# Performance work log

Measured on AMD Instinct MI355X. Metric: run time of the kernel, lower is better.

## Reference

```python
import jax, jax.numpy as jnp
import numpy as np

HIDDEN = 5120
HEAD_DIM = 128
HQ = 40
HKV = 8
NUM_MOD = 3
Q_SIZE = HQ * HEAD_DIM          # 5120
KV_SIZE = HKV * HEAD_DIM        # 1024
GATE = HQ                       # attn gating enabled
QKV_OUT = Q_SIZE + 2 * KV_SIZE + GATE  # 7208
EPS = 1e-6
N_TOK = 2048


def setup_inputs() -> dict:
    key = jax.random.key(0)
    ks = jax.random.split(key, 8)
    s = 0.02
    return {
        "hidden_states": jax.random.normal(ks[0], (N_TOK, HIDDEN), jnp.float32),
        "rope": jax.random.normal(ks[1], (N_TOK, HEAD_DIM), jnp.float32),
        "pre_norm_w": jax.random.normal(ks[2], (NUM_MOD * HIDDEN,), jnp.float32) * s,
        "qkv_w": jax.random.normal(ks[3], (NUM_MOD * QKV_OUT, HIDDEN), jnp.float32) * s,
        "q_norm_w": jax.random.normal(ks[4], (NUM_MOD * HEAD_DIM,), jnp.float32) * s,
        "k_norm_w": jax.random.normal(ks[5], (NUM_MOD * HEAD_DIM,), jnp.float32) * s,
        "proj_w": jax.random.normal(ks[6], (NUM_MOD * HIDDEN, Q_SIZE), jnp.float32) * s,
        "modality_ids": jax.random.randint(ks[7], (N_TOK,), 0, NUM_MOD, jnp.int64),
    }


def _mm_rmsnorm(x, w_flat, mids, dim):
    # per-token modality weight slice; residual parameterization (w + 1)
    w = w_flat.reshape(NUM_MOD, dim)[mids]  # [N, dim]
    if x.ndim == 3:
        w = w[:, None, :]  # broadcast over heads
    rms = jax.lax.rsqrt(jnp.mean(x * x, axis=-1, keepdims=True) + EPS)
    return x * rms * (w + 1.0)


def _moe_linear(x, w_flat, mids, out_f):
    # 3 GEMMs (one per expert), then per-token select -- same math as masked dispatch
    wm = w_flat.reshape(NUM_MOD, out_f, x.shape[-1])
    outs = jnp.einsum('nd,mod->nmo', x, wm)  # [N, 3, out_f]
    return jnp.take_along_axis(outs, mids[:, None, None], axis=1)[:, 0, :]


def _rotary(x, cos, sin):
    # x: [N, H, D]; cos/sin: [N, D/2]
    x1, x2 = jnp.split(x, 2, axis=-1)
    c = cos[:, None, :]
    s = sin[:, None, :]
    return jnp.concatenate([x1 * c - x2 * s, x1 * s + x2 * c], axis=-1)


def reference(hidden_states, rope, pre_norm_w, qkv_w, q_norm_w, k_norm_w, proj_w, modality_ids):
    N = hidden_states.shape[0]
    mids = modality_ids

    h = _mm_rmsnorm(hidden_states, pre_norm_w, mids, HIDDEN)
    qkv = _moe_linear(h, qkv_w, mids, QKV_OUT)  # [N, 7208]
    q, k, v, g = jnp.split(qkv, [Q_SIZE, Q_SIZE + KV_SIZE, Q_SIZE + 2 * KV_SIZE], axis=-1)
    q = q.reshape(N, HQ, HEAD_DIM)
    k = k.reshape(N, HKV, HEAD_DIM)
    v = v.reshape(N, HKV, HEAD_DIM)

    q = _mm_rmsnorm(q, q_norm_w, mids, HEAD_DIM)
    k = _mm_rmsnorm(k, k_norm_w, mids, HEAD_DIM)

    sin, cos = jnp.split(rope, 2, axis=-1)  # rope.chunk(2, dim=-1) -> sin, cos
    q = _rotary(q, cos, sin)
    k = _rotary(k, cos, sin)

    # GQA attention over the full token sequence
    G = HQ // HKV
    qg = q.reshape(N, HKV, G, HEAD_DIM)
    scale = 1.0 / np.sqrt(HEAD_DIM).astype(np.float32)
    scores = jnp.einsum('nkgd,mkd->kgnm', qg, k) * scale  # [8, 5, N, N]
    p = jax.nn.softmax(scores, axis=-1)
    o = jnp.einsum('kgnm,mkd->nkgd', p, v).reshape(N, HQ, HEAD_DIM)

    o = o * jax.nn.sigmoid(g)[:, :, None]  # attention gating per q-head
    o = o.reshape(N, Q_SIZE)
    return _moe_linear(o, proj_w, mids, HIDDEN)
```

## Files before the change

### kernel.cpp

```cpp
#include <hip/hip_runtime.h>
#include <hip/hip_bf16.h>

#define N_TOK 2048
#define HIDDEN 5120
#define HEAD_DIM 128
#define HQ 40
#define HKV 8
#define QKV_OUT 7208
#define Q_SIZE 5120
#define KV_SIZE 1024

typedef __attribute__((ext_vector_type(8))) short bf16x8;
typedef __attribute__((ext_vector_type(4))) float f32x4;
typedef __attribute__((ext_vector_type(4))) unsigned short us4;

__device__ inline unsigned short f2bf(float f) {
    return __builtin_bit_cast(unsigned short, __float2bfloat16(f));
}
__device__ inline float bf2f(unsigned short s) {
    unsigned u = ((unsigned)s) << 16;
    return __builtin_bit_cast(float, u);
}
__device__ inline f32x4 mfma16(bf16x8 a, bf16x8 b, f32x4 c) {
    return __builtin_amdgcn_mfma_f32_16x16x32_bf16(a, b, c, 0, 0, 0);
}
__device__ inline void gl16(const void* g, void* l) {
    __builtin_amdgcn_global_load_lds((__attribute__((address_space(1))) void*)g,
                                     (__attribute__((address_space(3))) void*)l, 16, 0, 0);
}

__global__ void k_sort(const int* __restrict__ mids_raw, int* __restrict__ meta,
                       int* __restrict__ perm) {
    int l = threadIdx.x;
    int oddnz = 0;
    for (int c = 0; c < 32; ++c) {
        int idx = c * 64 + l;
        int v = mids_raw[idx];
        if ((idx & 1) && v != 0) oddnz = 1;
    }
    bool is64 = (__ballot(oddnz) == 0ULL);
    int c0 = 0, c1 = 0;
    for (int c = 0; c < 32; ++c) {
        int i = c * 64 + l;
        int m = is64 ? mids_raw[2 * i] : mids_raw[i];
        c0 += (m == 0); c1 += (m == 1);
    }
    for (int o = 32; o; o >>= 1) { c0 += __shfl_xor(c0, o); c1 += __shfl_xor(c1, o); }
    if (l == 0) { meta[0] = 0; meta[1] = c0; meta[2] = c0 + c1; meta[3] = N_TOK; }
    int r0 = 0, r1 = c0, r2 = c0 + c1;
    unsigned long long below = (1ULL << l) - 1ULL;
    for (int c = 0; c < 32; ++c) {
        int i = c * 64 + l;
        int m = is64 ? mids_raw[2 * i] : mids_raw[i];
        unsigned long long b0 = __ballot(m == 0), b1 = __ballot(m == 1), b2 = __ballot(m == 2);
        int pos = (m == 0) ? r0 + __popcll(b0 & below)
                : (m == 1) ? r1 + __popcll(b1 & below)
                           : r2 + __popcll(b2 & below);
        perm[pos] = i;
        r0 += __popcll(b0); r1 += __popcll(b1); r2 += __popcll(b2);
    }
}

__global__ __launch_bounds__(256) void k_cvt(const float* __restrict__ src,
                                             unsigned short* __restrict__ dst, int n8) {
    int i = blockIdx.x * 256 + threadIdx.x;
    int stride = gridDim.x * 256;
    for (; i < n8; i += stride) {
        float4 a = ((const float4*)src)[2 * i];
        float4 b = ((const float4*)src)[2 * i + 1];
        bf16x8 o;
        o[0] = (short)f2bf(a.x); o[1] = (short)f2bf(a.y);
        o[2] = (short)f2bf(a.z); o[3] = (short)f2bf(a.w);
        o[4] = (short)f2bf(b.x); o[5] = (short)f2bf(b.y);
        o[6] = (short)f2bf(b.z); o[7] = (short)f2bf(b.w);
        ((bf16x8*)dst)[i] = o;
    }
}

__global__ __launch_bounds__(256) void k_prenorm(const float* __restrict__ hidden,
        const float* __restrict__ pnw, const int* __restrict__ meta,
        const int* __restrict__ perm, unsigned short* __restrict__ h) {
    int i = blockIdx.x;
    int m = (i >= meta[1]) + (i >= meta[2]);
    int t = perm[i];
    const float4* x = (const float4*)(hidden + (size_t)t * HIDDEN);
    const float4* wv = (const float4*)(pnw + (size_t)m * HIDDEN);
    int tid = threadIdx.x;
    float4 xv[5];
    float ss = 0.f;
#pragma unroll
    for (int j = 0; j < 5; ++j) {
        xv[j] = x[tid + j * 256];
        ss += xv[j].x * xv[j].x + xv[j].y * xv[j].y + xv[j].z * xv[j].z + xv[j].w * xv[j].w;
    }
    for (int o = 32; o; o >>= 1) ss += __shfl_xor(ss, o);
    __shared__ float red[4];
    if ((tid & 63) == 0) red[tid >> 6] = ss;
    __syncthreads();
    float rms = rsqrtf((red[0] + red[1] + red[2] + red[3]) * (1.f / HIDDEN) + 1e-6f);
    us4* dst = (us4*)(h + (size_t)i * HIDDEN);
#pragma unroll
    for (int j = 0; j < 5; ++j) {
        float4 w = wv[tid + j * 256];
        us4 o4;
        o4.x = f2bf(xv[j].x * rms * (w.x + 1.f));
        o4.y = f2bf(xv[j].y * rms * (w.y + 1.f));
        o4.z = f2bf(xv[j].z * rms * (w.z + 1.f));
        o4.w = f2bf(xv[j].w * rms * (w.w + 1.f));
        dst[tid + j * 256] = o4;
    }
}

template <int NOUT, bool SCATTER>
__global__ __launch_bounds__(256) void k_gemm(
        const unsigned short* __restrict__ A, const unsigned short* __restrict__ Bw,
        unsigned short* __restrict__ outB, float* __restrict__ outF,
        const int* __restrict__ meta, const int* __restrict__ perm,
        int nx, int ny) {
    int nwg = nx * ny * 3;
    int bid = blockIdx.x;
    int xcd = bid & 7, o = bid >> 3;
    int q = nwg >> 3, r = nwg & 7;
    int swz = (xcd < r ? xcd * (q + 1) : r * (q + 1) + (xcd - r) * q) + o;
    int mz = swz / (nx * ny);
    int rest = swz - mz * (nx * ny);
    int ty = rest / nx, tx = rest - ty * nx;

    int rowS = meta[mz], rowE = meta[mz + 1];
    int row0 = rowS + tx * 128;
    if (row0 >= rowE) return;
    int col0 = ty * 128;
    const unsigned short* Bm = Bw + (size_t)mz * NOUT * HIDDEN;

    __shared__ __align__(16) unsigned short As[128 * 64];
    __shared__ __align__(16) unsigned short Bs[128 * 64];
    int tid = threadIdx.x, l = tid & 63, w = tid >> 6;
    int wr = (w >> 1) * 64, wc = (w & 1) * 64;

    f32x4 acc[4][4] = {};

    const int lr = l >> 3, lc = l & 7;
    const int sch = (lc ^ lr) * 8;
    const unsigned short* ag[4];
    const unsigned short* bg[4];
#pragma unroll
    for (int j = 0; j < 4; ++j) {
        int ar = row0 + 32 * j + 8 * w + lr;
        if (ar > rowE - 1) ar = rowE - 1;
        ag[j] = A + (size_t)ar * HIDDEN + sch;
        int bc = col0 + 32 * j + 8 * w + lr;
        if (bc > NOUT - 1) bc = NOUT - 1;
        bg[j] = Bm + (size_t)bc * HIDDEN + sch;
    }
    char* asw = (char*)As + w * 1024;
    char* bsw = (char*)Bs + w * 1024;

#pragma unroll 1
    for (int kk = 0; kk < HIDDEN; kk += 64) {
#pragma unroll
        for (int j = 0; j < 4; ++j) {
            gl16(ag[j] + kk, asw + j * 4096);
            gl16(bg[j] + kk, bsw + j * 4096);
        }
        __syncthreads();
#pragma unroll
        for (int ks = 0; ks < 2; ++ks) {
            bf16x8 af[4], bfm[4];
#pragma unroll
            for (int mi = 0; mi < 4; ++mi) {
                int row = wr + mi * 16 + (l & 15);
                af[mi] = *(const bf16x8*)((char*)As + row * 128 +
                            ((ks * 64 + (l >> 4) * 16) ^ ((row & 7) << 4)));
            }
#pragma unroll
            for (int ni = 0; ni < 4; ++ni) {
                int row = wc + ni * 16 + (l & 15);
                bfm[ni] = *(const bf16x8*)((char*)Bs + row * 128 +
                            ((ks * 64 + (l >> 4) * 16) ^ ((row & 7) << 4)));
            }
#pragma unroll
            for (int mi = 0; mi < 4; ++mi)
#pragma unroll
                for (int ni = 0; ni < 4; ++ni)
                    acc[mi][ni] = mfma16(af[mi], bfm[ni], acc[mi][ni]);
        }
        __syncthreads();
    }
#pragma unroll
    for (int mi = 0; mi < 4; ++mi) {
        int rbase = row0 + wr + mi * 16 + ((l >> 4) << 2);
#pragma unroll
        for (int ni = 0; ni < 4; ++ni) {
            int col = col0 + wc + ni * 16 + (l & 15);
            if (col >= NOUT) continue;
#pragma unroll
            for (int rr = 0; rr < 4; ++rr) {
                int row = rbase + rr;
                if (row >= rowE) continue;
                if (SCATTER) {
                    int t = perm[row];
                    outF[(size_t)t * HIDDEN + col] = acc[mi][ni][rr];
                } else {
                    outB[(size_t)row * NOUT + col] = f2bf(acc[mi][ni][rr]);
                }
            }
        }
    }
}

template <int NOUT, bool SCATTER>
__global__ __launch_bounds__(256) void k_moe_gemm(
        const unsigned short* __restrict__ A, const float* __restrict__ B,
        unsigned short* __restrict__ outB, float* __restrict__ outF,
        const int* __restrict__ meta, const int* __restrict__ perm) {
    int mz = blockIdx.z;
    int rowS = meta[mz], rowE = meta[mz + 1];
    int row0 = rowS + blockIdx.y * 128;
    if (row0 >= rowE) return;
    int col0 = blockIdx.x * 128;
    const float* Bm = B + (size_t)mz * NOUT * HIDDEN;

    __shared__ __align__(16) unsigned short As[128 * 64];
    __shared__ __align__(16) unsigned short Bs[128 * 64];
    int tid = threadIdx.x, l = tid & 63, w = tid >> 6;
    int wr = (w >> 1) * 64, wc = (w & 1) * 64;

    f32x4 acc[4][4] = {};
    int sr = tid >> 1, half = tid & 1;
    int arow = row0 + sr;
    if (arow > N_TOK - 1) arow = N_TOK - 1;
    const unsigned short* aptr = A + (size_t)arow * HIDDEN + half * 32;
    int bcol = col0 + sr;
    bool bok = (bcol < NOUT);
    const float* bptr = Bm + (size_t)(bok ? bcol : 0) * HIDDEN + half * 32;

    char* awp[4]; char* bwp[4];
#pragma unroll
    for (int q = 0; q < 4; ++q) {
        int boff = sr * 128 + ((((half * 4 + q) * 16)) ^ ((sr & 7) << 4));
        awp[q] = (char*)As + boff;
        bwp[q] = (char*)Bs + boff;
    }

#pragma unroll 1
    for (int kk = 0; kk < HIDDEN; kk += 64) {
        bf16x8 av[4];
#pragma unroll
        for (int q = 0; q < 4; ++q) av[q] = *(const bf16x8*)(aptr + kk + q * 8);
        bf16x8 bw[4];
#pragma unroll
        for (int q = 0; q < 4; ++q) {
            float4 u, v;
            if (bok) {
                u = ((const float4*)(bptr + kk))[2 * q];
                v = ((const float4*)(bptr + kk))[2 * q + 1];
            } else {
                u = make_float4(0.f, 0.f, 0.f, 0.f);
                v = u;
            }
            bf16x8 pk;
            pk[0] = (short)f2bf(u.x); pk[1] = (short)f2bf(u.y);
            pk[2] = (short)f2bf(u.z); pk[3] = (short)f2bf(u.w);
            pk[4] = (short)f2bf(v.x); pk[5] = (short)f2bf(v.y);
            pk[6] = (short)f2bf(v.z); pk[7] = (short)f2bf(v.w);
            bw[q] = pk;
        }
        __syncthreads();
#pragma unroll
        for (int q = 0; q < 4; ++q) {
            *(bf16x8*)awp[q] = av[q];
            *(bf16x8*)bwp[q] = bw[q];
        }
        __syncthreads();
#pragma unroll
        for (int ks = 0; ks < 2; ++ks) {
            bf16x8 af[4], bfm[4];
#pragma unroll
            for (int mi = 0; mi < 4; ++mi) {
                int row = wr + mi * 16 + (l & 15);
                af[mi] = *(const bf16x8*)((char*)As + row * 128 +
                            ((ks * 64 + (l >> 4) * 16) ^ ((row & 7) << 4)));
            }
#pragma unroll
            for (int ni = 0; ni < 4; ++ni) {
                int row = wc + ni * 16 + (l & 15);
                bfm[ni] = *(const bf16x8*)((char*)Bs + row * 128 +
                            ((ks * 64 + (l >> 4) * 16) ^ ((row & 7) << 4)));
            }
#pragma unroll
            for (int mi = 0; mi < 4; ++mi)
#pragma unroll
                for (int ni = 0; ni < 4; ++ni)
                    acc[mi][ni] = mfma16(af[mi], bfm[ni], acc[mi][ni]);
        }
    }
#pragma unroll
    for (int mi = 0; mi < 4; ++mi) {
        int rbase = row0 + wr + mi * 16 + ((l >> 4) << 2);
#pragma unroll
        for (int ni = 0; ni < 4; ++ni) {
            int col = col0 + wc + ni * 16 + (l & 15);
            if (col >= NOUT) continue;
#pragma unroll
            for (int rr = 0; rr < 4; ++rr) {
                int row = rbase + rr;
                if (row >= rowE) continue;
                if (SCATTER) {
                    int t = perm[row];
                    outF[(size_t)t * HIDDEN + col] = acc[mi][ni][rr];
                } else {
                    outB[(size_t)row * NOUT + col] = f2bf(acc[mi][ni][rr]);
                }
            }
        }
    }
}

__global__ __launch_bounds__(256) void k_qknorm(const unsigned short* __restrict__ qkv,
        const float* __restrict__ rope, const float* __restrict__ qnw,
        const float* __restrict__ knw, const int* __restrict__ meta,
        const int* __restrict__ perm, unsigned short* __restrict__ qb,
        unsigned short* __restrict__ kb, float* __restrict__ gate) {
    int i = blockIdx.x;
    int m = (i >= meta[1]) + (i >= meta[2]);
    int t = perm[i];
    int tid = threadIdx.x, w = tid >> 6, l = tid & 63;
    const unsigned short* base = qkv + (size_t)i * QKV_OUT;
    const float* rp = rope + (size_t)t * HEAD_DIM;
    const float qscale = 0.08838834764831845f * 1.4426950408889634f;
    for (int hh = w; hh < 48; hh += 4) {
        bool isq = hh < 40;
        const unsigned short* src = base + (isq ? hh * 128 : Q_SIZE + (hh - 40) * 128);
        float x0 = bf2f(src[2 * l]), x1 = bf2f(src[2 * l + 1]);
        float ss = x0 * x0 + x1 * x1;
        for (int o = 32; o; o >>= 1) ss += __shfl_xor(ss, o);
        float rms = rsqrtf(ss * (1.f / 128.f) + 1e-6f);
        const float* nw = (isq ? qnw : knw) + m * 128;
        float y0 = x0 * rms * (nw[2 * l] + 1.f);
        float y1 = x1 * rms * (nw[2 * l + 1] + 1.f);
        float p0 = __shfl_xor(y0, 32);
        float p1 = __shfl_xor(y1, 32);
        float r0v, r1v;
        if (l < 32) {
            int d = 2 * l;
            r0v = y0 * rp[64 + d] - p0 * rp[d];
            r1v = y1 * rp[64 + d + 1] - p1 * rp[d + 1];
        } else {
            int d = 2 * l - 64;
            r0v = p0 * rp[d] + y0 * rp[64 + d];
            r1v = p1 * rp[d + 1] + y1 * rp[64 + d + 1];
        }
        if (isq) {
            r0v *= qscale; r1v *= qscale;
            unsigned short* dst = qb + (size_t)i * Q_SIZE + hh * 128 + 2 * l;
            dst[0] = f2bf(r0v); dst[1] = f2bf(r1v);
        } else {
            unsigned short* dst = kb + (size_t)i * KV_SIZE + (hh - 40) * 128 + 2 * l;
            dst[0] = f2bf(r0v); dst[1] = f2bf(r1v);
        }
    }
    if (tid < HQ) {
        float g = bf2f(base[Q_SIZE + 2 * KV_SIZE + tid]);
        gate[(size_t)i * HQ + tid] = 1.f / (1.f + expf(-g));
    }
}

__global__ __launch_bounds__(256) void k_vtrans(const unsigned short* __restrict__ qkv,
                                                unsigned short* __restrict__ vT) {
    int t0 = blockIdx.x * 64, db = blockIdx.y * 64, kvh = blockIdx.z;
    __shared__ unsigned short tile[64][68];
    int tid = threadIdx.x;
    int tr = tid >> 2, seg = tid & 3;
    const unsigned short* src = qkv + (size_t)(t0 + tr) * QKV_OUT + Q_SIZE + KV_SIZE +
                                kvh * 128 + db + seg * 16;
    us4* drow = (us4*)&tile[tr][seg * 16];
#pragma unroll
    for (int q = 0; q < 4; ++q) drow[q] = ((const us4*)src)[q];
    __syncthreads();
    int dr = tid >> 2;
    unsigned short* dst = vT + ((size_t)kvh * 128 + db + dr) * N_TOK + t0 + seg * 16;
    unsigned short buf[16];
#pragma unroll
    for (int j = 0; j < 16; ++j) buf[j] = tile[seg * 16 + j][dr];
#pragma unroll
    for (int q = 0; q < 4; ++q) ((us4*)dst)[q] = ((us4*)buf)[q];
}

__global__ __launch_bounds__(256) void k_attn(
        const unsigned short* __restrict__ qb,
        const unsigned short* __restrict__ kb,
        const unsigned short* __restrict__ vT,
        const float* __restrict__ gate,
        unsigned short* __restrict__ og) {
    int qt = blockIdx.x, qh = blockIdx.y, kvh = qh / 5;
    int tid = threadIdx.x, w = tid >> 6, l = tid & 63;
    int q0 = qt * 128 + w * 32;
    __shared__ __align__(16) char smem[49152];
    char* Ks = smem;
    char* Vs = smem + 16384;
    char* Ps = smem + 32768 + w * 4096;

    bf16x8 qf[2][4];
#pragma unroll
    for (int mi = 0; mi < 2; ++mi)
#pragma unroll
        for (int ks = 0; ks < 4; ++ks)
            qf[mi][ks] = *(const bf16x8*)(qb + (size_t)(q0 + mi * 16 + (l & 15)) * Q_SIZE +
                                          qh * 128 + ks * 32 + (l >> 4) * 8);

    f32x4 oacc[2][8] = {};
    f32x4 psum[2] = {};

    int kr = tid >> 2, kseg = tid & 3;
    int vr = tid >> 1, vh2 = tid & 1;

#pragma unroll 1
    for (int kt = 0; kt < 32; ++kt) {
        int t0 = kt * 64;
        bf16x8 kv4[4], vv4[4];
        const unsigned short* ksrc = kb + (size_t)(t0 + kr) * KV_SIZE + kvh * 128 + kseg * 32;
        const unsigned short* vsrc = vT + ((size_t)kvh * 128 + vr) * N_TOK + t0 + vh2 * 32;
#pragma unroll
        for (int q = 0; q < 4; ++q) {
            kv4[q] = *(const bf16x8*)(ksrc + q * 8);
            vv4[q] = *(const bf16x8*)(vsrc + q * 8);
        }
        __syncthreads();
#pragma unroll
        for (int q = 0; q < 4; ++q) {
            *(bf16x8*)(Ks + kr * 256 + ((((kseg * 4 + q) * 16)) ^ ((kr & 7) << 4))) = kv4[q];
            *(bf16x8*)(Vs + vr * 128 + ((((vh2 * 4 + q) * 16)) ^ ((vr & 7) << 4))) = vv4[q];
        }
        __syncthreads();
        f32x4 s[2][4] = {};
#pragma unroll
        for (int ks = 0; ks < 4; ++ks) {
            bf16x8 kf[4];
#pragma unroll
            for (int ni = 0; ni < 4; ++ni) {
                int row = ni * 16 + (l & 15);
                kf[ni] = *(const bf16x8*)(Ks + row * 256 +
                            ((ks * 64 + (l >> 4) * 16) ^ ((row & 7) << 4)));
            }
#pragma unroll
            for (int mi = 0; mi < 2; ++mi)
#pragma unroll
                for (int ni = 0; ni < 4; ++ni)
                    s[mi][ni] = mfma16(qf[mi][ks], kf[ni], s[mi][ni]);
        }
#pragma unroll
        for (int mi = 0; mi < 2; ++mi)
#pragma unroll
            for (int ni = 0; ni < 4; ++ni) {
#pragma unroll
                for (int r = 0; r < 4; ++r) {
                    float p = exp2f(s[mi][ni][r]);
                    psum[mi][r] += p;
                    int qr = mi * 16 + ((l >> 4) << 2) + r;
                    int tcb = (ni * 16 + (l & 15)) * 2;
                    *(unsigned short*)(Ps + qr * 128 +
                        (tcb ^ (((qr >> 2) & 3) << 5))) = f2bf(p);
                }
            }
#pragma unroll
        for (int ks = 0; ks < 2; ++ks) {
            bf16x8 pa[2];
#pragma unroll
            for (int mi = 0; mi < 2; ++mi) {
                int qr = mi * 16 + (l & 15);
                pa[mi] = *(const bf16x8*)(Ps + qr * 128 +
                            ((ks * 64 + (l >> 4) * 16) ^ (((qr >> 2) & 3) << 5)));
            }
#pragma unroll
            for (int nd = 0; nd < 8; ++nd) {
                int row = nd * 16 + (l & 15);
                bf16x8 vf = *(const bf16x8*)(Vs + row * 128 +
                            ((ks * 64 + (l >> 4) * 16) ^ ((row & 7) << 4)));
#pragma unroll
                for (int mi = 0; mi < 2; ++mi)
                    oacc[mi][nd] = mfma16(pa[mi], vf, oacc[mi][nd]);
            }
        }
    }
#pragma unroll
    for (int mi = 0; mi < 2; ++mi)
#pragma unroll
        for (int r = 0; r < 4; ++r) {
            float v = psum[mi][r];
            v += __shfl_xor(v, 1);
            v += __shfl_xor(v, 2);
            v += __shfl_xor(v, 4);
            v += __shfl_xor(v, 8);
            psum[mi][r] = v;
        }
#pragma unroll
    for (int mi = 0; mi < 2; ++mi)
#pragma unroll
        for (int r = 0; r < 4; ++r) {
            int row = q0 + mi * 16 + ((l >> 4) << 2) + r;
            float sc = (1.f / psum[mi][r]) * gate[(size_t)row * HQ + qh];
#pragma unroll
            for (int nd = 0; nd < 8; ++nd)
                og[(size_t)row * Q_SIZE + qh * 128 + nd * 16 + (l & 15)] =
                    f2bf(oacc[mi][nd][r] * sc);
        }
}

extern "C" void kernel_launch(void* const* d_in, const int* in_sizes, int n_in,
                              void* d_out, int out_size, void* d_ws, size_t ws_size,
                              hipStream_t stream) {
    const float* hidden = (const float*)d_in[0];
    const float* rope   = (const float*)d_in[1];
    const float* pnw    = (const float*)d_in[2];
    const float* qkvw   = (const float*)d_in[3];
    const float* qnw    = (const float*)d_in[4];
    const float* knw    = (const float*)d_in[5];
    const float* projw  = (const float*)d_in[6];
    const int*   mids   = (const int*)d_in[7];
    float* out = (float*)d_out;

    char* ws = (char*)d_ws;
    const size_t nqkvw = (size_t)3 * QKV_OUT * HIDDEN;
    const size_t nprojw = (size_t)3 * HIDDEN * Q_SIZE;
    const size_t wbytes = (nqkvw + nprojw) * 2;

    const size_t small_bytes = 16384 +
        (size_t)N_TOK * HIDDEN * 2 +
        (size_t)N_TOK * QKV_OUT * 2 +
        (size_t)N_TOK * Q_SIZE * 2 +
        (size_t)N_TOK * KV_SIZE * 2 +
        (size_t)N_TOK * KV_SIZE * 2 +
        (size_t)N_TOK * Q_SIZE * 2 +
        (size_t)N_TOK * HQ * 4;
    bool use_bf = (ws_size >= wbytes + small_bytes);
    if (!use_bf && ws_size < small_bytes) return;

    unsigned short* wqkv = (unsigned short*)ws;
    unsigned short* wproj = wqkv + nqkvw;
    char* sb = ws + (use_bf ? wbytes : 0);

    int* meta = (int*)sb;
    int* perm = (int*)(sb + 64);
    unsigned short* h   = (unsigned short*)(sb + 16384);
    unsigned short* qkv = h   + (size_t)N_TOK * HIDDEN;
    unsigned short* qb  = qkv + (size_t)N_TOK * QKV_OUT;
    unsigned short* kb  = qb  + (size_t)N_TOK * Q_SIZE;
    unsigned short* vT  = kb  + (size_t)N_TOK * KV_SIZE;
    unsigned short* og  = vT  + (size_t)N_TOK * KV_SIZE;
    float* gate = (float*)(og + (size_t)N_TOK * Q_SIZE);

    k_sort<<<1, 64, 0, stream>>>(mids, meta, perm);
    if (use_bf) {
        k_cvt<<<2048, 256, 0, stream>>>(qkvw, wqkv, (int)(nqkvw / 8));
        k_cvt<<<2048, 256, 0, stream>>>(projw, wproj, (int)(nprojw / 8));
    }
    k_prenorm<<<2048, 256, 0, stream>>>(hidden, pnw, meta, perm, h);
    if (use_bf)
        k_gemm<QKV_OUT, false><<<16 * 57 * 3, 256, 0, stream>>>(
            h, wqkv, qkv, nullptr, meta, perm, 16, 57);
    else
        k_moe_gemm<QKV_OUT, false><<<dim3(57, 16, 3), 256, 0, stream>>>(
            h, qkvw, qkv, nullptr, meta, perm);
    k_qknorm<<<2048, 256, 0, stream>>>(qkv, rope, qnw, knw, meta, perm, qb, kb, gate);
    k_vtrans<<<dim3(32, 2, 8), 256, 0, stream>>>(qkv, vT);
    k_attn<<<dim3(16, 40), 256, 0, stream>>>(qb, kb, vT, gate, og);
    if (use_bf)
        k_gemm<HIDDEN, true><<<16 * 40 * 3, 256, 0, stream>>>(
            og, wproj, nullptr, out, meta, perm, 16, 40);
    else
        k_moe_gemm<HIDDEN, true><<<dim3(40, 16, 3), 256, 0, stream>>>(
            og, projw, nullptr, out, meta, perm);
}
```

Before: 1.076 ms.

## Use 256x256 GEMM tiles, fuse weight conversion into other kernels, prefetch attention K/V

The bf16 GEMM moves from 128x128 tiles on 256 threads to 256x256 tiles on 512 threads with 8x4 accumulators per wave, so each loaded byte feeds more MFMA work. The QKV weight conversion now runs in extra blocks of the pre-norm kernel, and the projection weight conversion runs in extra blocks of the QKV GEMM, which removes two separate launches. The attention kernel prefetches the next K/V tile into registers while computing the current one. The cost is higher register and LDS pressure, fewer GEMM blocks (possible wave-quantisation loss on small modality groups), and conversion blocks that compete with the main work for compute units.

```diff
diff --git a/kernel.cpp b/kernel.cpp
--- a/kernel.cpp
+++ b/kernel.cpp
@@ -27,6 +27,20 @@
 __device__ inline void gl16(const void* g, void* l) {
     __builtin_amdgcn_global_load_lds((__attribute__((address_space(1))) void*)g,
                                      (__attribute__((address_space(3))) void*)l, 16, 0, 0);
+}
+__device__ inline void cvt_chunk(const float* __restrict__ src,
+                                 unsigned short* __restrict__ dst,
+                                 int n8, int i, int stride) {
+    for (; i < n8; i += stride) {
+        float4 a = ((const float4*)src)[2 * i];
+        float4 b = ((const float4*)src)[2 * i + 1];
+        bf16x8 o;
+        o[0] = (short)f2bf(a.x); o[1] = (short)f2bf(a.y);
+        o[2] = (short)f2bf(a.z); o[3] = (short)f2bf(a.w);
+        o[4] = (short)f2bf(b.x); o[5] = (short)f2bf(b.y);
+        o[6] = (short)f2bf(b.z); o[7] = (short)f2bf(b.w);
+        ((bf16x8*)dst)[i] = o;
+    }
 }
 
 __global__ void k_sort(const int* __restrict__ mids_raw, int* __restrict__ meta,
@@ -61,31 +75,23 @@
     }
 }
 
-__global__ __launch_bounds__(256) void k_cvt(const float* __restrict__ src,
-                                             unsigned short* __restrict__ dst, int n8) {
-    int i = blockIdx.x * 256 + threadIdx.x;
-    int stride = gridDim.x * 256;
-    for (; i < n8; i += stride) {
-        float4 a = ((const float4*)src)[2 * i];
-        float4 b = ((const float4*)src)[2 * i + 1];
-        bf16x8 o;
-        o[0] = (short)f2bf(a.x); o[1] = (short)f2bf(a.y);
-        o[2] = (short)f2bf(a.z); o[3] = (short)f2bf(a.w);
-        o[4] = (short)f2bf(b.x); o[5] = (short)f2bf(b.y);
-        o[6] = (short)f2bf(b.z); o[7] = (short)f2bf(b.w);
-        ((bf16x8*)dst)[i] = o;
-    }
-}
-
-__global__ __launch_bounds__(256) void k_prenorm(const float* __restrict__ hidden,
+__global__ __launch_bounds__(256) void k_prenorm_cvt(const float* __restrict__ hidden,
         const float* __restrict__ pnw, const int* __restrict__ meta,
-        const int* __restrict__ perm, unsigned short* __restrict__ h) {
-    int i = blockIdx.x;
+        const int* __restrict__ perm, unsigned short* __restrict__ h,
+        const float* __restrict__ csrc, unsigned short* __restrict__ cdst, int n8) {
+    int bid = blockIdx.x;
+    int tid = threadIdx.x;
+    if (bid >= 2048) {
+        int b = bid - 2048;
+        int stride = (gridDim.x - 2048) * 256;
+        cvt_chunk(csrc, cdst, n8, b * 256 + tid, stride);
+        return;
+    }
+    int i = bid;
     int m = (i >= meta[1]) + (i >= meta[2]);
     int t = perm[i];
     const float4* x = (const float4*)(hidden + (size_t)t * HIDDEN);
     const float4* wv = (const float4*)(pnw + (size_t)m * HIDDEN);
-    int tid = threadIdx.x;
     float4 xv[5];
     float ss = 0.f;
 #pragma unroll
@@ -112,13 +118,21 @@
 }
 
 template <int NOUT, bool SCATTER>
-__global__ __launch_bounds__(256) void k_gemm(
+__global__ __launch_bounds__(512, 2) void k_g256(
         const unsigned short* __restrict__ A, const unsigned short* __restrict__ Bw,
         unsigned short* __restrict__ outB, float* __restrict__ outF,
         const int* __restrict__ meta, const int* __restrict__ perm,
-        int nx, int ny) {
+        int nx, int ny,
+        const float* __restrict__ csrc, unsigned short* __restrict__ cdst, int n8) {
     int nwg = nx * ny * 3;
     int bid = blockIdx.x;
+    int tid = threadIdx.x;
+    if (bid >= nwg) {
+        int b = bid - nwg;
+        int stride = (gridDim.x - nwg) * 512;
+        cvt_chunk(csrc, cdst, n8, b * 512 + tid, stride);
+        return;
+    }
     int xcd = bid & 7, o = bid >> 3;
     int q = nwg >> 3, r = nwg & 7;
     int swz = (xcd < r ? xcd * (q + 1) : r * (q + 1) + (xcd - r) * q) + o;
@@ -127,17 +141,17 @@
     int ty = rest / nx, tx = rest - ty * nx;
 
     int rowS = meta[mz], rowE = meta[mz + 1];
-    int row0 = rowS + tx * 128;
+    int row0 = rowS + tx * 256;
     if (row0 >= rowE) return;
-    int col0 = ty * 128;
+    int col0 = ty * 256;
     const unsigned short* Bm = Bw + (size_t)mz * NOUT * HIDDEN;
 
-    __shared__ __align__(16) unsigned short As[128 * 64];
-    __shared__ __align__(16) unsigned short Bs[128 * 64];
-    int tid = threadIdx.x, l = tid & 63, w = tid >> 6;
-    int wr = (w >> 1) * 64, wc = (w & 1) * 64;
-
-    f32x4 acc[4][4] = {};
+    __shared__ __align__(16) unsigned short As[256 * 64];
+    __shared__ __align__(16) unsigned short Bs[256 * 64];
+    int l = tid & 63, w = tid >> 6;
+    int wr = (w >> 2) * 128, wc = (w & 3) * 64;
+
+    f32x4 acc[8][4] = {};
 
     const int lr = l >> 3, lc = l & 7;
     const int sch = (lc ^ lr) * 8;
@@ -145,10 +159,10 @@
     const unsigned short* bg[4];
 #pragma unroll
     for (int j = 0; j < 4; ++j) {
-        int ar = row0 + 32 * j + 8 * w + lr;
+        int ar = row0 + 64 * j + 8 * w + lr;
         if (ar > rowE - 1) ar = rowE - 1;
         ag[j] = A + (size_t)ar * HIDDEN + sch;
-        int bc = col0 + 32 * j + 8 * w + lr;
+        int bc = col0 + 64 * j + 8 * w + lr;
         if (bc > NOUT - 1) bc = NOUT - 1;
         bg[j] = Bm + (size_t)bc * HIDDEN + sch;
     }
@@ -158,16 +172,15 @@
 #pragma unroll 1
     for (int kk = 0; kk < HIDDEN; kk += 64) {
 #pragma unroll
-        for (int j = 0; j < 4; ++j) {
-            gl16(ag[j] + kk, asw + j * 4096);
-            gl16(bg[j] + kk, bsw + j * 4096);
-        }
+        for (int j = 0; j < 4; ++j) gl16(ag[j] + kk, asw + j * 8192);
+#pragma unroll
+        for (int j = 0; j < 4; ++j) gl16(bg[j] + kk, bsw + j * 8192);
         __syncthreads();
 #pragma unroll
         for (int ks = 0; ks < 2; ++ks) {
-            bf16x8 af[4], bfm[4];
-#pragma unroll
-            for (int mi = 0; mi < 4; ++mi) {
+            bf16x8 af[8], bfm[4];
+#pragma unroll
+            for (int mi = 0; mi < 8; ++mi) {
                 int row = wr + mi * 16 + (l & 15);
                 af[mi] = *(const bf16x8*)((char*)As + row * 128 +
                             ((ks * 64 + (l >> 4) * 16) ^ ((row & 7) << 4)));
@@ -179,7 +192,7 @@
                             ((ks * 64 + (l >> 4) * 16) ^ ((row & 7) << 4)));
             }
 #pragma unroll
-            for (int mi = 0; mi < 4; ++mi)
+            for (int mi = 0; mi < 8; ++mi)
 #pragma unroll
                 for (int ni = 0; ni < 4; ++ni)
                     acc[mi][ni] = mfma16(af[mi], bfm[ni], acc[mi][ni]);
@@ -187,7 +200,7 @@
         __syncthreads();
     }
 #pragma unroll
-    for (int mi = 0; mi < 4; ++mi) {
+    for (int mi = 0; mi < 8; ++mi) {
         int rbase = row0 + wr + mi * 16 + ((l >> 4) << 2);
 #pragma unroll
         for (int ni = 0; ni < 4; ++ni) {
@@ -392,8 +405,10 @@
         const unsigned short* __restrict__ vT,
         const float* __restrict__ gate,
         unsigned short* __restrict__ og) {
-    int qt = blockIdx.x, qh = blockIdx.y, kvh = qh / 5;
-    int tid = threadIdx.x, w = tid >> 6, l = tid & 63;
+    int bid = blockIdx.x;
+    int tid = threadIdx.x;
+    int qt = bid & 15, qh = bid >> 4, kvh = qh / 5;
+    int w = tid >> 6, l = tid & 63;
     int q0 = qt * 128 + w * 32;
     __shared__ __align__(16) char smem[49152];
     char* Ks = smem;
@@ -413,18 +428,18 @@
 
     int kr = tid >> 2, kseg = tid & 3;
     int vr = tid >> 1, vh2 = tid & 1;
+    const unsigned short* ksrc0 = kb + (size_t)kr * KV_SIZE + kvh * 128 + kseg * 32;
+    const unsigned short* vsrc0 = vT + ((size_t)kvh * 128 + vr) * N_TOK + vh2 * 32;
+
+    bf16x8 kv4[4], vv4[4];
+#pragma unroll
+    for (int q = 0; q < 4; ++q) {
+        kv4[q] = *(const bf16x8*)(ksrc0 + q * 8);
+        vv4[q] = *(const bf16x8*)(vsrc0 + q * 8);
+    }
 
 #pragma unroll 1
     for (int kt = 0; kt < 32; ++kt) {
-        int t0 = kt * 64;
-        bf16x8 kv4[4], vv4[4];
-        const unsigned short* ksrc = kb + (size_t)(t0 + kr) * KV_SIZE + kvh * 128 + kseg * 32;
-        const unsigned short* vsrc = vT + ((size_t)kvh * 128 + vr) * N_TOK + t0 + vh2 * 32;
-#pragma unroll
-        for (int q = 0; q < 4; ++q) {
-            kv4[q] = *(const bf16x8*)(ksrc + q * 8);
-            vv4[q] = *(const bf16x8*)(vsrc + q * 8);
-        }
         __syncthreads();
 #pragma unroll
         for (int q = 0; q < 4; ++q) {
@@ -432,6 +447,15 @@
             *(bf16x8*)(Vs + vr * 128 + ((((vh2 * 4 + q) * 16)) ^ ((vr & 7) << 4))) = vv4[q];
         }
         __syncthreads();
+        if (kt + 1 < 32) {
+            const unsigned short* ksrc = ksrc0 + (size_t)(kt + 1) * 64 * KV_SIZE;
+            const unsigned short* vsrc = vsrc0 + (kt + 1) * 64;
+#pragma unroll
+            for (int q = 0; q < 4; ++q) {
+                kv4[q] = *(const bf16x8*)(ksrc + q * 8);
+                vv4[q] = *(const bf16x8*)(vsrc + q * 8);
+            }
+        }
         f32x4 s[2][4] = {};
 #pragma unroll
         for (int ks = 0; ks < 4; ++ks) {
@@ -551,23 +575,26 @@
 
     k_sort<<<1, 64, 0, stream>>>(mids, meta, perm);
     if (use_bf) {
-        k_cvt<<<2048, 256, 0, stream>>>(qkvw, wqkv, (int)(nqkvw / 8));
-        k_cvt<<<2048, 256, 0, stream>>>(projw, wproj, (int)(nprojw / 8));
-    }
-    k_prenorm<<<2048, 256, 0, stream>>>(hidden, pnw, meta, perm, h);
-    if (use_bf)
-        k_gemm<QKV_OUT, false><<<16 * 57 * 3, 256, 0, stream>>>(
-            h, wqkv, qkv, nullptr, meta, perm, 16, 57);
-    else
+        k_prenorm_cvt<<<2048 + 1024, 256, 0, stream>>>(
+            hidden, pnw, meta, perm, h, qkvw, wqkv, (int)(nqkvw / 8));
+        k_g256<QKV_OUT, false><<<8 * 29 * 3 + 512, 512, 0, stream>>>(
+            h, wqkv, qkv, nullptr, meta, perm, 8, 29,
+            projw, wproj, (int)(nprojw / 8));
+        k_qknorm<<<2048, 256, 0, stream>>>(qkv, rope, qnw, knw, meta, perm, qb, kb, gate);
+        k_vtrans<<<dim3(32, 2, 8), 256, 0, stream>>>(qkv, vT);
+        k_attn<<<640, 256, 0, stream>>>(qb, kb, vT, gate, og);
+        k_g256<HIDDEN, true><<<8 * 20 * 3, 512, 0, stream>>>(
+            og, wproj, nullptr, out, meta, perm, 8, 20,
+            nullptr, nullptr, 0);
+    } else {
+        k_prenorm_cvt<<<2048, 256, 0, stream>>>(
+            hidden, pnw, meta, perm, h, nullptr, nullptr, 0);
         k_moe_gemm<QKV_OUT, false><<<dim3(57, 16, 3), 256, 0, stream>>>(
             h, qkvw, qkv, nullptr, meta, perm);
-    k_qknorm<<<2048, 256, 0, stream>>>(qkv, rope, qnw, knw, meta, perm, qb, kb, gate);
-    k_vtrans<<<dim3(32, 2, 8), 256, 0, stream>>>(qkv, vT);
-    k_attn<<<dim3(16, 40), 256, 0, stream>>>(qb, kb, vT, gate, og);
-    if (use_bf)
-        k_gemm<HIDDEN, true><<<16 * 40 * 3, 256, 0, stream>>>(
-            og, wproj, nullptr, out, meta, perm, 16, 40);
-    else
+        k_qknorm<<<2048, 256, 0, stream>>>(qkv, rope, qnw, knw, meta, perm, qb, kb, gate);
+        k_vtrans<<<dim3(32, 2, 8), 256, 0, stream>>>(qkv, vT);
+        k_attn<<<640, 256, 0, stream>>>(qb, kb, vT, gate, og);
         k_moe_gemm<HIDDEN, true><<<dim3(40, 16, 3), 256, 0, stream>>>(
             og, projw, nullptr, out, meta, perm);
-}
+    }
+}
```

Result: faster. 1.012 ms (-6.0%).
